# Kernel tuning notes

Measured on AMD Instinct MI355X. Metric: run time of the kernel, lower is better.

The kernel has to match this reference:

```python
import jax, jax.numpy as jnp
import numpy as np

N_NODES = 10000
N_EDGES = 640000
IN_FEAT = 128
HIDDEN = 128
CLASSES = 2
NEG_SLOPE = 0.2


def glorot(key, shape):
    lim = float(np.sqrt(6.0 / (shape[0] + shape[-1])))
    return jax.random.uniform(key, shape, jnp.float32, -lim, lim)


def setup_inputs() -> dict:
    key = jax.random.key(0)
    ks = jax.random.split(key, 10)
    x = jax.random.normal(ks[0], (N_NODES, IN_FEAT), jnp.float32)
    edge_index = jax.random.randint(ks[1], (2, N_EDGES), 0, N_NODES, jnp.int64)
    return {
        "x": x,
        "edge_index": edge_index,
        "W1": glorot(ks[2], (IN_FEAT, HIDDEN)),
        "a_src1": glorot(ks[3], (HIDDEN, 1))[:, 0],
        "a_dst1": glorot(ks[4], (HIDDEN, 1))[:, 0],
        "b1": jnp.zeros((HIDDEN,), jnp.float32),
        "W2": glorot(ks[5], (HIDDEN, CLASSES)),
        "a_src2": glorot(ks[6], (CLASSES, 1))[:, 0],
        "a_dst2": glorot(ks[7], (CLASSES, 1))[:, 0],
        "b2": jnp.zeros((CLASSES,), jnp.float32),
    }


def gat_conv(x, src, dst, W, a_src, a_dst, b, n_nodes):
    # x: [N, Fin] -> h: [N, Fout]
    h = x @ W
    # per-node attention logits (single head)
    alpha_s = h @ a_src  # [N]
    alpha_d = h @ a_dst  # [N]
    e = jax.nn.leaky_relu(alpha_s[src] + alpha_d[dst], NEG_SLOPE)  # [E]
    # segment softmax over incoming edges of each dst node
    m = jax.ops.segment_max(e, dst, num_segments=n_nodes)
    ex = jnp.exp(e - m[dst])
    denom = jax.ops.segment_sum(ex, dst, num_segments=n_nodes)
    w = ex / denom[dst]  # [E]
    # weighted scatter-aggregate of source messages
    out = jax.ops.segment_sum(h[src] * w[:, None], dst, num_segments=n_nodes)
    return out + b


def reference(x, edge_index, W1, a_src1, a_dst1, b1, W2, a_src2, a_dst2, b2):
    n = x.shape[0]
    # PyG GATConv default: add self-loops
    loops = jnp.arange(n, dtype=edge_index.dtype)
    src = jnp.concatenate([edge_index[0], loops])
    dst = jnp.concatenate([edge_index[1], loops])
    h = gat_conv(x, src, dst, W1, a_src1, a_dst1, b1, n)
    h = jax.nn.relu(h)
    out = gat_conv(h, src, dst, W2, a_src2, a_dst2, b2, n)
    return out
```

## Files before the change

### kernel.cpp

```cpp
#include <hip/hip_runtime.h>
#include <hip/hip_bf16.h>

#define NN 10000
#define NE 640000
#define ETOT (NE + NN)
#define FEAT 128
#define NEG 0.2f
#define CAP 160
#define NBUCK 157
#define BCAP 5120
#define EPB 4096
#define NB1 ((ETOT + EPB - 1) / EPB)
#define GEMM_ROWS 16
#define NBG (NN / GEMM_ROWS)
#define NJOB1 (NB1 + NBG)
#define NJAGG ((NN + 3) / 4)

typedef short bf16x8 __attribute__((ext_vector_type(8)));
typedef float f32x4  __attribute__((ext_vector_type(4)));

__device__ __forceinline__ short f2bf(float f) {
    unsigned u = __float_as_uint(f);
    unsigned r = (u + 0x7FFFu + ((u >> 16) & 1u)) >> 16;
    return (short)r;
}

union ShMem {
    struct {
        int hist[160]; int scan[256]; int excl[160]; int cursor[160]; int base[160];
        unsigned int pairs[EPB];
    } p;
};

__device__ __forceinline__ int detect64(const void* ep) {
    const unsigned long long* p64 = (const unsigned long long*)ep;
    unsigned long long v = p64[threadIdx.x & 63];
    unsigned long long bal = __ballot((v >> 32) != 0ULL);
    return (bal == 0ULL) ? 1 : 0;
}

__global__ __launch_bounds__(256) void prep_kernel(
        const float* __restrict__ W1, const float* __restrict__ a_src1,
        const float* __restrict__ a_dst1,
        unsigned short* __restrict__ W1t, float* __restrict__ wa, float* __restrict__ wd,
        int* __restrict__ gbcnt) {
    int idx = blockIdx.x * 256 + threadIdx.x;
    if (idx < FEAT * FEAT) {
        int n = idx >> 7, k = idx & 127;
        W1t[n * FEAT + k] = (unsigned short)f2bf(W1[k * FEAT + n]);
    }
    int i2 = idx - FEAT * FEAT;
    if (i2 >= 0 && i2 < NBUCK * 16) gbcnt[i2] = 0;
    int i3 = idx - (FEAT * FEAT + NBUCK * 16);
    if (i3 >= 0 && i3 < FEAT) {
        float s = 0.f;
        for (int k = 0; k < FEAT; k++) s += W1[i3 * FEAT + k] * a_src1[k];
        wa[i3] = s;
    } else if (i3 >= FEAT && i3 < 2 * FEAT) {
        int j = i3 - FEAT;
        float s = 0.f;
        for (int k = 0; k < FEAT; k++) s += W1[j * FEAT + k] * a_dst1[k];
        wd[j] = s;
    }
}

__device__ __forceinline__ void bin_job(const void* ep, int flag64,
        int* __restrict__ gbcnt, unsigned int* __restrict__ staged,
        ShMem& sh, int tid, int job) {
    for (int i = tid; i < 160; i += 256) sh.p.hist[i] = 0;
    __syncthreads();
    const int e0 = job * EPB;
    int nE = ETOT - e0; if (nE > EPB) nE = EPB;
    const bool full = (nE == EPB);
    unsigned int key[16];
    if (full) {
#pragma unroll
        for (int k = 0; k < 16; k++) {
            int e = e0 + tid + k * 256, s, d;
            if (e < NE) {
                if (flag64) { const long long* p = (const long long*)ep; s = (int)p[e]; d = (int)p[NE + e]; }
                else        { const int* p = (const int*)ep;       s = p[e];       d = p[NE + e]; }
            } else { s = e - NE; d = s; }
            key[k] = ((unsigned)d << 14) | (unsigned)s;
            atomicAdd(&sh.p.hist[d >> 6], 1);
        }
    } else {
        for (int k = 0; k < 16; k++) {
            int idx = tid + k * 256;
            if (idx < nE) {
                int e = e0 + idx, s, d;
                if (e < NE) {
                    if (flag64) { const long long* p = (const long long*)ep; s = (int)p[e]; d = (int)p[NE + e]; }
                    else        { const int* p = (const int*)ep;       s = p[e];       d = p[NE + e]; }
                } else { s = e - NE; d = s; }
                atomicAdd(&sh.p.hist[d >> 6], 1);
            }
        }
    }
    __syncthreads();
    sh.p.scan[tid] = (tid < 160) ? sh.p.hist[tid] : 0;
    __syncthreads();
    for (int off = 1; off < 256; off <<= 1) {
        int t = (tid >= off) ? sh.p.scan[tid - off] : 0;
        __syncthreads();
        sh.p.scan[tid] += t;
        __syncthreads();
    }
    if (tid < 160) {
        int ex = sh.p.scan[tid] - sh.p.hist[tid];
        sh.p.excl[tid] = ex;
        sh.p.cursor[tid] = ex;
        sh.p.base[tid] = (tid < NBUCK && sh.p.hist[tid] > 0)
                           ? atomicAdd(&gbcnt[tid * 16], sh.p.hist[tid]) : 0;
    }
    __syncthreads();
    if (full) {
#pragma unroll
        for (int k = 0; k < 16; k++) {
            int b = key[k] >> 20;
            int pos = atomicAdd(&sh.p.cursor[b], 1);
            sh.p.pairs[pos] = key[k];
        }
    } else {
        for (int k = 0; k < 16; k++) {
            int idx = tid + k * 256;
            if (idx < nE) {
                int e = e0 + idx, s, d;
                if (e < NE) {
                    if (flag64) { const long long* p = (const long long*)ep; s = (int)p[e]; d = (int)p[NE + e]; }
                    else        { const int* p = (const int*)ep;       s = p[e];       d = p[NE + e]; }
                } else { s = e - NE; d = s; }
                unsigned int kk = ((unsigned)d << 14) | (unsigned)s;
                int pos = atomicAdd(&sh.p.cursor[d >> 6], 1);
                sh.p.pairs[pos] = kk;
            }
        }
    }
    __syncthreads();
    for (int i = tid; i < nE; i += 256) {
        unsigned int kk = sh.p.pairs[i];
        int b = kk >> 20;
        int idx = sh.p.base[b] + (i - sh.p.excl[b]);
        if (idx < BCAP) staged[b * BCAP + idx] = kk;
    }
}

__device__ __forceinline__ void gemm_job(
        const float* __restrict__ x, const unsigned short* __restrict__ W1t,
        const float* __restrict__ wa, const float* __restrict__ wd,
        unsigned short* __restrict__ h1, float* __restrict__ as1, float* __restrict__ ad1,
        int tid, int gb) {
    const int row0 = gb * GEMM_ROWS;
    const int lane = tid & 63, wv = tid >> 6;
    const int m = lane & 15, g = lane >> 4;
    const int n0 = wv * 32;
    const float* arow = x + (size_t)(row0 + m) * FEAT + g * 8;
    const unsigned short* bb0 = W1t + (size_t)(n0 + m) * FEAT + g * 8;
    const unsigned short* bb1 = W1t + (size_t)(n0 + 16 + m) * FEAT + g * 8;
    const bool do_logit = (wv == 0);
    f32x4 acc0 = {0.f, 0.f, 0.f, 0.f}, acc1 = {0.f, 0.f, 0.f, 0.f};
    float la = 0.f, ld = 0.f;
#pragma unroll
    for (int kt = 0; kt < 4; kt++) {
        float4 v0 = *(const float4*)(arow + kt * 32);
        float4 v1 = *(const float4*)(arow + kt * 32 + 4);
        if (do_logit) {
            float4 wa0 = *(const float4*)(wa + g * 8 + kt * 32);
            float4 wa1 = *(const float4*)(wa + g * 8 + kt * 32 + 4);
            float4 wd0 = *(const float4*)(wd + g * 8 + kt * 32);
            float4 wd1 = *(const float4*)(wd + g * 8 + kt * 32 + 4);
            la += v0.x * wa0.x + v0.y * wa0.y + v0.z * wa0.z + v0.w * wa0.w
                + v1.x * wa1.x + v1.y * wa1.y + v1.z * wa1.z + v1.w * wa1.w;
            ld += v0.x * wd0.x + v0.y * wd0.y + v0.z * wd0.z + v0.w * wd0.w
                + v1.x * wd1.x + v1.y * wd1.y + v1.z * wd1.z + v1.w * wd1.w;
        }
        bf16x8 a;
        a[0] = f2bf(v0.x); a[1] = f2bf(v0.y); a[2] = f2bf(v0.z); a[3] = f2bf(v0.w);
        a[4] = f2bf(v1.x); a[5] = f2bf(v1.y); a[6] = f2bf(v1.z); a[7] = f2bf(v1.w);
        bf16x8 b0 = *(const bf16x8*)(bb0 + kt * 32);
        bf16x8 b1 = *(const bf16x8*)(bb1 + kt * 32);
        acc0 = __builtin_amdgcn_mfma_f32_16x16x32_bf16(a, b0, acc0, 0, 0, 0);
        acc1 = __builtin_amdgcn_mfma_f32_16x16x32_bf16(a, b1, acc1, 0, 0, 0);
    }
    if (do_logit) {
        la += __shfl_xor(la, 16); la += __shfl_xor(la, 32);
        ld += __shfl_xor(ld, 16); ld += __shfl_xor(ld, 32);
        if (g == 0) { as1[row0 + m] = la; ad1[row0 + m] = ld; }
    }
#pragma unroll
    for (int r = 0; r < 4; r++) {
        int row = row0 + g * 4 + r;
        h1[(size_t)row * FEAT + n0 + m]      = (unsigned short)f2bf(acc0[r]);
        h1[(size_t)row * FEAT + n0 + 16 + m] = (unsigned short)f2bf(acc1[r]);
    }
}

__global__ __launch_bounds__(256) void fat1_kernel(const void* ep,
        const float* __restrict__ x, const unsigned short* __restrict__ W1t,
        const float* __restrict__ wa, const float* __restrict__ wd,
        int* __restrict__ gbcnt, unsigned int* __restrict__ staged,
        unsigned short* __restrict__ h1, float* __restrict__ as1, float* __restrict__ ad1) {
    __shared__ ShMem sh;
    int blk = blockIdx.x, tid = threadIdx.x;
    if (blk < NB1) { int f = detect64(ep); bin_job(ep, f, gbcnt, staged, sh, tid, blk); }
    else gemm_job(x, W1t, wa, wd, h1, as1, ad1, tid, blk - NB1);
}

__global__ __launch_bounds__(256) void scatter2_kernel(const int* __restrict__ gbcnt,
        const unsigned int* __restrict__ staged, int* __restrict__ slots, int* __restrict__ deg) {
    __shared__ int ncnt[64];
    int b = blockIdx.x, tid = threadIdx.x;
    if (tid < 64) ncnt[tid] = 0;
    __syncthreads();
    int total = gbcnt[b * 16]; if (total > BCAP) total = BCAP;
    for (int i = tid; i < total; i += 256) {
        unsigned int kk = staged[b * BCAP + i];
        int d = kk >> 14, s = kk & 0x3FFF;
        int lp = atomicAdd(&ncnt[d & 63], 1);
        if (lp < CAP) slots[d * CAP + lp] = s;
    }
    __syncthreads();
    if (tid < 64) {
        int node = b * 64 + tid;
        if (node < NN) deg[node] = min(ncnt[tid], CAP);
    }
}

__global__ __launch_bounds__(256) void agg1_kernel(const int* __restrict__ deg,
        const int* __restrict__ slots, const float* __restrict__ as1,
        const float* __restrict__ ad1, const unsigned int* __restrict__ h1u,
        const float* __restrict__ b1, const float* __restrict__ W2,
        const float* __restrict__ a_src2, const float* __restrict__ a_dst2,
        float* __restrict__ h2, float* __restrict__ as2, float* __restrict__ ad2) {
    __shared__ float2 ws_s[4][CAP];
    int tid = threadIdx.x;
    int wi = tid >> 6, lane = tid & 63;
    int v = blockIdx.x * 4 + wi;
    if (v >= NN) return;
    int c = deg[v];
    const int base = v * CAP;
    float adv = ad1[v];

    int i0 = lane, i1 = lane + 64, i2 = lane + 128;
    float dsum = 0.f;
    if (i0 < c) {
        int s = slots[base + i0];
        float t = as1[s] + adv; t = (t > 0.f) ? t : NEG * t;
        float w = __expf(fminf(t, 80.f));
        ws_s[wi][i0] = make_float2(w, __int_as_float(s)); dsum += w;
    }
    if (i1 < c) {
        int s = slots[base + i1];
        float t = as1[s] + adv; t = (t > 0.f) ? t : NEG * t;
        float w = __expf(fminf(t, 80.f));
        ws_s[wi][i1] = make_float2(w, __int_as_float(s)); dsum += w;
    }
    if (i2 < c) {
        int s = slots[base + i2];
        float t = as1[s] + adv; t = (t > 0.f) ? t : NEG * t;
        float w = __expf(fminf(t, 80.f));
        ws_s[wi][i2] = make_float2(w, __int_as_float(s)); dsum += w;
    }
#pragma unroll
    for (int o = 32; o; o >>= 1) dsum += __shfl_xor(dsum, o);

    float ax = 0.f, ay = 0.f;
#pragma unroll 4
    for (int i = 0; i < c; i++) {
        float2 ws = ws_s[wi][i];
        float wgt = ws.x;
        int s = __float_as_int(ws.y);
        unsigned int u = h1u[s * 64 + lane];
        ax += wgt * __uint_as_float(u << 16);
        ay += wgt * __uint_as_float(u & 0xFFFF0000u);
    }
    float inv = 1.f / dsum;
    float2 bb = ((const float2*)b1)[lane];
    float hx = fmaxf(ax * inv + bb.x, 0.f);
    float hy = fmaxf(ay * inv + bb.y, 0.f);

    const float2* w2p = (const float2*)W2;
    float2 wc0 = w2p[2 * lane], wc1 = w2p[2 * lane + 1];
    float c0 = hx * wc0.x + hy * wc1.x;
    float c1 = hx * wc0.y + hy * wc1.y;
#pragma unroll
    for (int o = 32; o; o >>= 1) { c0 += __shfl_down(c0, o); c1 += __shfl_down(c1, o); }
    if (lane == 0) {
        ((float2*)h2)[v] = make_float2(c0, c1);
        as2[v] = c0 * a_src2[0] + c1 * a_src2[1];
        ad2[v] = c0 * a_dst2[0] + c1 * a_dst2[1];
    }
}

__global__ __launch_bounds__(256) void agg2_kernel(const int* __restrict__ deg,
        const int* __restrict__ slots, const float* __restrict__ as2,
        const float* __restrict__ ad2, const float* __restrict__ h2,
        const float* __restrict__ b2, float* __restrict__ out) {
    int tid = threadIdx.x;
    int wi = tid >> 6, lane = tid & 63;
    int v = blockIdx.x * 4 + wi;
    if (v >= NN) return;
    int c = deg[v];
    int base = v * CAP;
    float adv = ad2[v];
    float dsum = 0.f, a0 = 0.f, a1 = 0.f;
    for (int i = lane; i < c; i += 64) {
        int s = slots[base + i];
        float e = as2[s] + adv;
        e = (e > 0.f) ? e : NEG * e;
        float w = __expf(fminf(e, 80.f));
        dsum += w;
        float2 hv = ((const float2*)h2)[s];
        a0 += w * hv.x; a1 += w * hv.y;
    }
#pragma unroll
    for (int o = 32; o; o >>= 1) {
        dsum += __shfl_xor(dsum, o);
        a0 += __shfl_xor(a0, o);
        a1 += __shfl_xor(a1, o);
    }
    if (lane == 0) {
        out[v * 2]     = a0 / dsum + b2[0];
        out[v * 2 + 1] = a1 / dsum + b2[1];
    }
}

extern "C" void kernel_launch(void* const* d_in, const int* in_sizes, int n_in,
                              void* d_out, int out_size, void* d_ws, size_t ws_size,
                              hipStream_t stream) {
    const float* x      = (const float*)d_in[0];
    const void*  edges  = d_in[1];
    const float* W1     = (const float*)d_in[2];
    const float* a_src1 = (const float*)d_in[3];
    const float* a_dst1 = (const float*)d_in[4];
    const float* b1     = (const float*)d_in[5];
    const float* W2     = (const float*)d_in[6];
    const float* a_src2 = (const float*)d_in[7];
    const float* a_dst2 = (const float*)d_in[8];
    const float* b2     = (const float*)d_in[9];
    float* out = (float*)d_out;

    char* w = (char*)d_ws;
    size_t off = 0;
    auto alloc = [&](size_t bytes) { void* p = w + off; off += (bytes + 255) & ~size_t(255); return p; };
    int*             gbcnt  = (int*)alloc((size_t)NBUCK * 16 * 4);
    unsigned int*    staged = (unsigned int*)alloc((size_t)NBUCK * BCAP * 4);
    int*             slots  = (int*)alloc((size_t)NN * CAP * 4);
    int*             deg    = (int*)alloc((size_t)NN * 4);
    unsigned short*  h1     = (unsigned short*)alloc((size_t)NN * FEAT * 2);
    unsigned short*  W1t    = (unsigned short*)alloc((size_t)FEAT * FEAT * 2);
    float*           wa     = (float*)alloc(FEAT * 4);
    float*           wd     = (float*)alloc(FEAT * 4);
    float*           as1    = (float*)alloc(NN * 4);
    float*           ad1    = (float*)alloc(NN * 4);
    float*           h2     = (float*)alloc(NN * 2 * 4);
    float*           as2    = (float*)alloc(NN * 4);
    float*           ad2    = (float*)alloc(NN * 4);

    int prep_items = FEAT * FEAT + NBUCK * 16 + 2 * FEAT;
    prep_kernel<<<(prep_items + 255) / 256, 256, 0, stream>>>(W1, a_src1, a_dst1,
                                                              W1t, wa, wd, gbcnt);
    fat1_kernel<<<NJOB1, 256, 0, stream>>>(edges, x, W1t, wa, wd,
                                           gbcnt, staged, h1, as1, ad1);
    scatter2_kernel<<<NBUCK, 256, 0, stream>>>(gbcnt, staged, slots, deg);
    agg1_kernel<<<NJAGG, 256, 0, stream>>>(deg, slots, as1, ad1,
                                           (const unsigned int*)h1, b1,
                                           W2, a_src2, a_dst2, h2, as2, ad2);
    agg2_kernel<<<NJAGG, 256, 0, stream>>>(deg, slots, as2, ad2, h2, b2, out);
}
```

Measured before the change: 60.16 us.

## Fuse bucket scatter into layer-1 aggregation by rescanning staged buckets per block

Removes the separate scatter kernel. Each aggregation block of 4 destination nodes now scans its whole 64-node staged bucket, keeps only the edges for its own nodes, and builds the weight lists and softmax denominators in shared memory using atomics. It then writes slots and deg for use by layer 2. This saves one launch and the slots round trip through global memory, but every bucket is now read 16 times, and the order of edges and the float summation order change from run to run.

```diff
diff --git a/kernel.cpp b/kernel.cpp
--- a/kernel.cpp
+++ b/kernel.cpp
@@ -206,68 +206,46 @@
     else gemm_job(x, W1t, wa, wd, h1, as1, ad1, tid, blk - NB1);
 }
 
-__global__ __launch_bounds__(256) void scatter2_kernel(const int* __restrict__ gbcnt,
-        const unsigned int* __restrict__ staged, int* __restrict__ slots, int* __restrict__ deg) {
-    __shared__ int ncnt[64];
-    int b = blockIdx.x, tid = threadIdx.x;
-    if (tid < 64) ncnt[tid] = 0;
-    __syncthreads();
+__global__ __launch_bounds__(256) void agg1scan_kernel(const int* __restrict__ gbcnt,
+        const unsigned int* __restrict__ staged, const float* __restrict__ as1,
+        const float* __restrict__ ad1, const unsigned int* __restrict__ h1u,
+        const float* __restrict__ b1, const float* __restrict__ W2,
+        const float* __restrict__ a_src2, const float* __restrict__ a_dst2,
+        int* __restrict__ slots, int* __restrict__ deg,
+        float* __restrict__ h2, float* __restrict__ as2, float* __restrict__ ad2) {
+    __shared__ float2 lists[4][CAP];
+    __shared__ int   cnt[4];
+    __shared__ float dsumS[4];
+    int j = blockIdx.x, tid = threadIdx.x;
+    int b = (4 * j) >> 6;
+    if (tid < 4) { cnt[tid] = 0; dsumS[tid] = 0.f; }
+    __syncthreads();
+
     int total = gbcnt[b * 16]; if (total > BCAP) total = BCAP;
     for (int i = tid; i < total; i += 256) {
         unsigned int kk = staged[b * BCAP + i];
-        int d = kk >> 14, s = kk & 0x3FFF;
-        int lp = atomicAdd(&ncnt[d & 63], 1);
-        if (lp < CAP) slots[d * CAP + lp] = s;
-    }
-    __syncthreads();
-    if (tid < 64) {
-        int node = b * 64 + tid;
-        if (node < NN) deg[node] = min(ncnt[tid], CAP);
-    }
-}
-
-__global__ __launch_bounds__(256) void agg1_kernel(const int* __restrict__ deg,
-        const int* __restrict__ slots, const float* __restrict__ as1,
-        const float* __restrict__ ad1, const unsigned int* __restrict__ h1u,
-        const float* __restrict__ b1, const float* __restrict__ W2,
-        const float* __restrict__ a_src2, const float* __restrict__ a_dst2,
-        float* __restrict__ h2, float* __restrict__ as2, float* __restrict__ ad2) {
-    __shared__ float2 ws_s[4][CAP];
-    int tid = threadIdx.x;
+        int d = kk >> 14;
+        if ((d >> 2) == j) {
+            int s = kk & 0x3FFF;
+            int nl = d & 3;
+            float t = as1[s] + ad1[d];
+            t = (t > 0.f) ? t : NEG * t;
+            float w = __expf(fminf(t, 80.f));
+            int lp = atomicAdd(&cnt[nl], 1);
+            atomicAdd(&dsumS[nl], w);
+            if (lp < CAP) lists[nl][lp] = make_float2(w, __int_as_float(s));
+        }
+    }
+    __syncthreads();
+
     int wi = tid >> 6, lane = tid & 63;
-    int v = blockIdx.x * 4 + wi;
-    if (v >= NN) return;
-    int c = deg[v];
-    const int base = v * CAP;
-    float adv = ad1[v];
-
-    int i0 = lane, i1 = lane + 64, i2 = lane + 128;
-    float dsum = 0.f;
-    if (i0 < c) {
-        int s = slots[base + i0];
-        float t = as1[s] + adv; t = (t > 0.f) ? t : NEG * t;
-        float w = __expf(fminf(t, 80.f));
-        ws_s[wi][i0] = make_float2(w, __int_as_float(s)); dsum += w;
-    }
-    if (i1 < c) {
-        int s = slots[base + i1];
-        float t = as1[s] + adv; t = (t > 0.f) ? t : NEG * t;
-        float w = __expf(fminf(t, 80.f));
-        ws_s[wi][i1] = make_float2(w, __int_as_float(s)); dsum += w;
-    }
-    if (i2 < c) {
-        int s = slots[base + i2];
-        float t = as1[s] + adv; t = (t > 0.f) ? t : NEG * t;
-        float w = __expf(fminf(t, 80.f));
-        ws_s[wi][i2] = make_float2(w, __int_as_float(s)); dsum += w;
-    }
-#pragma unroll
-    for (int o = 32; o; o >>= 1) dsum += __shfl_xor(dsum, o);
-
+    int v = 4 * j + wi;
+    int c = min(cnt[wi], CAP);
+    float dsum = dsumS[wi];
     float ax = 0.f, ay = 0.f;
 #pragma unroll 4
     for (int i = 0; i < c; i++) {
-        float2 ws = ws_s[wi][i];
+        float2 ws = lists[wi][i];
         float wgt = ws.x;
         int s = __float_as_int(ws.y);
         unsigned int u = h1u[s * 64 + lane];
@@ -289,7 +267,10 @@
         ((float2*)h2)[v] = make_float2(c0, c1);
         as2[v] = c0 * a_src2[0] + c1 * a_src2[1];
         ad2[v] = c0 * a_dst2[0] + c1 * a_dst2[1];
-    }
+        deg[v] = c;
+    }
+    for (int i = lane; i < c; i += 64)
+        slots[v * CAP + i] = __float_as_int(lists[wi][i].y);
 }
 
 __global__ __launch_bounds__(256) void agg2_kernel(const int* __restrict__ deg,
@@ -362,9 +343,9 @@
                                                               W1t, wa, wd, gbcnt);
     fat1_kernel<<<NJOB1, 256, 0, stream>>>(edges, x, W1t, wa, wd,
                                            gbcnt, staged, h1, as1, ad1);
-    scatter2_kernel<<<NBUCK, 256, 0, stream>>>(gbcnt, staged, slots, deg);
-    agg1_kernel<<<NJAGG, 256, 0, stream>>>(deg, slots, as1, ad1,
-                                           (const unsigned int*)h1, b1,
-                                           W2, a_src2, a_dst2, h2, as2, ad2);
+    agg1scan_kernel<<<NJAGG, 256, 0, stream>>>(gbcnt, staged, as1, ad1,
+                                               (const unsigned int*)h1, b1,
+                                               W2, a_src2, a_dst2,
+                                               slots, deg, h2, as2, ad2);
     agg2_kernel<<<NJAGG, 256, 0, stream>>>(deg, slots, as2, ad2, h2, b2, out);
 }
```

Result: slower. 69.32 us (+15.2%).

## Remove prep kernel; use per-job staging slots instead of global bucket atomics

Applied to the files above, without the earlier changes.

Drops the separate prep launch. Each GEMM block now recomputes the W1·a logit vectors into shared memory and reads and converts W1 columns straight from fp32 instead of using a pre-transposed bf16 copy. Edge binning no longer takes global atomic offsets per bucket. Each (bucket, job) pair writes to a fixed 96-entry slot with its own count, and scatter2 runs 1024-thread blocks that walk these segments. This removes one launch, the need to zero counters, and global atomic contention. In exchange, every GEMM block repeats a 128x128 dot-product setup and does strided uncoalesced W1 loads, and any (bucket, job) holding more than 96 edges is silently truncated.

```diff
diff --git a/kernel.cpp b/kernel.cpp
--- a/kernel.cpp
+++ b/kernel.cpp
@@ -8,9 +8,9 @@
 #define NEG 0.2f
 #define CAP 160
 #define NBUCK 157
-#define BCAP 5120
 #define EPB 4096
 #define NB1 ((ETOT + EPB - 1) / EPB)
+#define JSLOT 96
 #define GEMM_ROWS 16
 #define NBG (NN / GEMM_ROWS)
 #define NJOB1 (NB1 + NBG)
@@ -27,9 +27,10 @@
 
 union ShMem {
     struct {
-        int hist[160]; int scan[256]; int excl[160]; int cursor[160]; int base[160];
+        int hist[160]; int scan[256]; int excl[160]; int cursor[160];
         unsigned int pairs[EPB];
     } p;
+    struct { float wal[FEAT]; float wdl[FEAT]; } g;
 };
 
 __device__ __forceinline__ int detect64(const void* ep) {
@@ -39,33 +40,8 @@
     return (bal == 0ULL) ? 1 : 0;
 }
 
-__global__ __launch_bounds__(256) void prep_kernel(
-        const float* __restrict__ W1, const float* __restrict__ a_src1,
-        const float* __restrict__ a_dst1,
-        unsigned short* __restrict__ W1t, float* __restrict__ wa, float* __restrict__ wd,
-        int* __restrict__ gbcnt) {
-    int idx = blockIdx.x * 256 + threadIdx.x;
-    if (idx < FEAT * FEAT) {
-        int n = idx >> 7, k = idx & 127;
-        W1t[n * FEAT + k] = (unsigned short)f2bf(W1[k * FEAT + n]);
-    }
-    int i2 = idx - FEAT * FEAT;
-    if (i2 >= 0 && i2 < NBUCK * 16) gbcnt[i2] = 0;
-    int i3 = idx - (FEAT * FEAT + NBUCK * 16);
-    if (i3 >= 0 && i3 < FEAT) {
-        float s = 0.f;
-        for (int k = 0; k < FEAT; k++) s += W1[i3 * FEAT + k] * a_src1[k];
-        wa[i3] = s;
-    } else if (i3 >= FEAT && i3 < 2 * FEAT) {
-        int j = i3 - FEAT;
-        float s = 0.f;
-        for (int k = 0; k < FEAT; k++) s += W1[j * FEAT + k] * a_dst1[k];
-        wd[j] = s;
-    }
-}
-
 __device__ __forceinline__ void bin_job(const void* ep, int flag64,
-        int* __restrict__ gbcnt, unsigned int* __restrict__ staged,
+        unsigned int* __restrict__ staged, int* __restrict__ jcnt,
         ShMem& sh, int tid, int job) {
     for (int i = tid; i < 160; i += 256) sh.p.hist[i] = 0;
     __syncthreads();
@@ -110,8 +86,7 @@
         int ex = sh.p.scan[tid] - sh.p.hist[tid];
         sh.p.excl[tid] = ex;
         sh.p.cursor[tid] = ex;
-        sh.p.base[tid] = (tid < NBUCK && sh.p.hist[tid] > 0)
-                           ? atomicAdd(&gbcnt[tid * 16], sh.p.hist[tid]) : 0;
+        if (tid < NBUCK) jcnt[tid * NB1 + job] = min(sh.p.hist[tid], JSLOT);
     }
     __syncthreads();
     if (full) {
@@ -140,23 +115,34 @@
     for (int i = tid; i < nE; i += 256) {
         unsigned int kk = sh.p.pairs[i];
         int b = kk >> 20;
-        int idx = sh.p.base[b] + (i - sh.p.excl[b]);
-        if (idx < BCAP) staged[b * BCAP + idx] = kk;
+        int pos = i - sh.p.excl[b];
+        if (pos < JSLOT) staged[(size_t)(b * NB1 + job) * JSLOT + pos] = kk;
     }
 }
 
 __device__ __forceinline__ void gemm_job(
-        const float* __restrict__ x, const unsigned short* __restrict__ W1t,
-        const float* __restrict__ wa, const float* __restrict__ wd,
+        const float* __restrict__ x, const float* __restrict__ W1,
+        const float* __restrict__ a_src1, const float* __restrict__ a_dst1,
         unsigned short* __restrict__ h1, float* __restrict__ as1, float* __restrict__ ad1,
-        int tid, int gb) {
+        ShMem& sh, int tid, int gb) {
     const int row0 = gb * GEMM_ROWS;
     const int lane = tid & 63, wv = tid >> 6;
     const int m = lane & 15, g = lane >> 4;
     const int n0 = wv * 32;
+
+    {
+        int jj = tid & 127;
+        const float* wrow = W1 + (size_t)jj * FEAT;
+        const float* avec = (tid < 128) ? a_src1 : a_dst1;
+        float acc = 0.f;
+        for (int k = 0; k < FEAT; k++) acc += wrow[k] * avec[k];
+        if (tid < 128) sh.g.wal[jj] = acc; else sh.g.wdl[jj] = acc;
+    }
+    __syncthreads();
+
     const float* arow = x + (size_t)(row0 + m) * FEAT + g * 8;
-    const unsigned short* bb0 = W1t + (size_t)(n0 + m) * FEAT + g * 8;
-    const unsigned short* bb1 = W1t + (size_t)(n0 + 16 + m) * FEAT + g * 8;
+    const float* w1c0 = W1 + n0 + m;
+    const float* w1c1 = W1 + n0 + 16 + m;
     const bool do_logit = (wv == 0);
     f32x4 acc0 = {0.f, 0.f, 0.f, 0.f}, acc1 = {0.f, 0.f, 0.f, 0.f};
     float la = 0.f, ld = 0.f;
@@ -165,20 +151,23 @@
         float4 v0 = *(const float4*)(arow + kt * 32);
         float4 v1 = *(const float4*)(arow + kt * 32 + 4);
         if (do_logit) {
-            float4 wa0 = *(const float4*)(wa + g * 8 + kt * 32);
-            float4 wa1 = *(const float4*)(wa + g * 8 + kt * 32 + 4);
-            float4 wd0 = *(const float4*)(wd + g * 8 + kt * 32);
-            float4 wd1 = *(const float4*)(wd + g * 8 + kt * 32 + 4);
-            la += v0.x * wa0.x + v0.y * wa0.y + v0.z * wa0.z + v0.w * wa0.w
-                + v1.x * wa1.x + v1.y * wa1.y + v1.z * wa1.z + v1.w * wa1.w;
-            ld += v0.x * wd0.x + v0.y * wd0.y + v0.z * wd0.z + v0.w * wd0.w
-                + v1.x * wd1.x + v1.y * wd1.y + v1.z * wd1.z + v1.w * wd1.w;
+            const float* wap = sh.g.wal + g * 8 + kt * 32;
+            const float* wdp = sh.g.wdl + g * 8 + kt * 32;
+            la += v0.x * wap[0] + v0.y * wap[1] + v0.z * wap[2] + v0.w * wap[3]
+                + v1.x * wap[4] + v1.y * wap[5] + v1.z * wap[6] + v1.w * wap[7];
+            ld += v0.x * wdp[0] + v0.y * wdp[1] + v0.z * wdp[2] + v0.w * wdp[3]
+                + v1.x * wdp[4] + v1.y * wdp[5] + v1.z * wdp[6] + v1.w * wdp[7];
         }
         bf16x8 a;
         a[0] = f2bf(v0.x); a[1] = f2bf(v0.y); a[2] = f2bf(v0.z); a[3] = f2bf(v0.w);
         a[4] = f2bf(v1.x); a[5] = f2bf(v1.y); a[6] = f2bf(v1.z); a[7] = f2bf(v1.w);
-        bf16x8 b0 = *(const bf16x8*)(bb0 + kt * 32);
-        bf16x8 b1 = *(const bf16x8*)(bb1 + kt * 32);
+        bf16x8 b0, b1;
+#pragma unroll
+        for (int i = 0; i < 8; i++) {
+            int k = kt * 32 + g * 8 + i;
+            b0[i] = f2bf(w1c0[(size_t)k * FEAT]);
+            b1[i] = f2bf(w1c1[(size_t)k * FEAT]);
+        }
         acc0 = __builtin_amdgcn_mfma_f32_16x16x32_bf16(a, b0, acc0, 0, 0, 0);
         acc1 = __builtin_amdgcn_mfma_f32_16x16x32_bf16(a, b1, acc1, 0, 0, 0);
     }
@@ -196,28 +185,34 @@
 }
 
 __global__ __launch_bounds__(256) void fat1_kernel(const void* ep,
-        const float* __restrict__ x, const unsigned short* __restrict__ W1t,
-        const float* __restrict__ wa, const float* __restrict__ wd,
-        int* __restrict__ gbcnt, unsigned int* __restrict__ staged,
+        const float* __restrict__ x, const float* __restrict__ W1,
+        const float* __restrict__ a_src1, const float* __restrict__ a_dst1,
+        unsigned int* __restrict__ staged, int* __restrict__ jcnt,
         unsigned short* __restrict__ h1, float* __restrict__ as1, float* __restrict__ ad1) {
     __shared__ ShMem sh;
     int blk = blockIdx.x, tid = threadIdx.x;
-    if (blk < NB1) { int f = detect64(ep); bin_job(ep, f, gbcnt, staged, sh, tid, blk); }
-    else gemm_job(x, W1t, wa, wd, h1, as1, ad1, tid, blk - NB1);
-}
-
-__global__ __launch_bounds__(256) void scatter2_kernel(const int* __restrict__ gbcnt,
+    if (blk < NB1) { int f = detect64(ep); bin_job(ep, f, staged, jcnt, sh, tid, blk); }
+    else gemm_job(x, W1, a_src1, a_dst1, h1, as1, ad1, sh, tid, blk - NB1);
+}
+
+__global__ __launch_bounds__(1024) void scatter2_kernel(const int* __restrict__ jcnt,
         const unsigned int* __restrict__ staged, int* __restrict__ slots, int* __restrict__ deg) {
+    __shared__ int cnt_s[NB1];
     __shared__ int ncnt[64];
     int b = blockIdx.x, tid = threadIdx.x;
     if (tid < 64) ncnt[tid] = 0;
-    __syncthreads();
-    int total = gbcnt[b * 16]; if (total > BCAP) total = BCAP;
-    for (int i = tid; i < total; i += 256) {
-        unsigned int kk = staged[b * BCAP + i];
-        int d = kk >> 14, s = kk & 0x3FFF;
-        int lp = atomicAdd(&ncnt[d & 63], 1);
-        if (lp < CAP) slots[d * CAP + lp] = s;
+    for (int j = tid; j < NB1; j += 1024) cnt_s[j] = jcnt[b * NB1 + j];
+    __syncthreads();
+    int wv = tid >> 6, lane = tid & 63;
+    for (int j = wv; j < NB1; j += 16) {
+        int c = cnt_s[j];
+        const unsigned int* seg = staged + (size_t)(b * NB1 + j) * JSLOT;
+        for (int i = lane; i < c; i += 64) {
+            unsigned int kk = seg[i];
+            int d = kk >> 14, s = kk & 0x3FFF;
+            int lp = atomicAdd(&ncnt[d & 63], 1);
+            if (lp < CAP) slots[d * CAP + lp] = s;
+        }
     }
     __syncthreads();
     if (tid < 64) {
@@ -343,26 +338,20 @@
     char* w = (char*)d_ws;
     size_t off = 0;
     auto alloc = [&](size_t bytes) { void* p = w + off; off += (bytes + 255) & ~size_t(255); return p; };
-    int*             gbcnt  = (int*)alloc((size_t)NBUCK * 16 * 4);
-    unsigned int*    staged = (unsigned int*)alloc((size_t)NBUCK * BCAP * 4);
+    unsigned int*    staged = (unsigned int*)alloc((size_t)NBUCK * NB1 * JSLOT * 4);
+    int*             jcnt   = (int*)alloc((size_t)NBUCK * NB1 * 4);
     int*             slots  = (int*)alloc((size_t)NN * CAP * 4);
     int*             deg    = (int*)alloc((size_t)NN * 4);
     unsigned short*  h1     = (unsigned short*)alloc((size_t)NN * FEAT * 2);
-    unsigned short*  W1t    = (unsigned short*)alloc((size_t)FEAT * FEAT * 2);
-    float*           wa     = (float*)alloc(FEAT * 4);
-    float*           wd     = (float*)alloc(FEAT * 4);
     float*           as1    = (float*)alloc(NN * 4);
     float*           ad1    = (float*)alloc(NN * 4);
     float*           h2     = (float*)alloc(NN * 2 * 4);
     float*           as2    = (float*)alloc(NN * 4);
     float*           ad2    = (float*)alloc(NN * 4);
 
-    int prep_items = FEAT * FEAT + NBUCK * 16 + 2 * FEAT;
-    prep_kernel<<<(prep_items + 255) / 256, 256, 0, stream>>>(W1, a_src1, a_dst1,
-                                                              W1t, wa, wd, gbcnt);
-    fat1_kernel<<<NJOB1, 256, 0, stream>>>(edges, x, W1t, wa, wd,
-                                           gbcnt, staged, h1, as1, ad1);
-    scatter2_kernel<<<NBUCK, 256, 0, stream>>>(gbcnt, staged, slots, deg);
+    fat1_kernel<<<NJOB1, 256, 0, stream>>>(edges, x, W1, a_src1, a_dst1,
+                                           staged, jcnt, h1, as1, ad1);
+    scatter2_kernel<<<NBUCK, 1024, 0, stream>>>(jcnt, staged, slots, deg);
     agg1_kernel<<<NJAGG, 256, 0, stream>>>(deg, slots, as1, ad1,
                                            (const unsigned int*)h1, b1,
                                            W2, a_src2, a_dst2, h2, as2, ad2);
```

New measurement: 60.06 us (median of 2 runs). Within noise of the previous version (-0.2%).
